# Performance work log

Measured on AMD Instinct MI355X. Metric: run time of the kernel, lower is better.

## Reference

```python
import jax, jax.numpy as jnp
import numpy as np

T, D, H, E, K = 8192, 1024, 1024, 8, 2
N = T * K  # total dispatched rows


def setup_inputs() -> dict:
    key = jax.random.key(0)
    ks = jax.random.split(key, 12)
    s = 1.0 / np.sqrt(D)
    inp = {
        # uniform, contiguous per-expert segments: 2048 rows each
        'offsets': jnp.arange(E + 1, dtype=jnp.int64 if jax.config.jax_enable_x64 else jnp.int32) * (N // E),
        'jagged': jax.random.normal(ks[0], (T, D), jnp.float32),
        'weight': jax.random.normal(ks[1], (E, D, H), jnp.float32) * s,
        'bias': jax.random.normal(ks[2], (E, H), jnp.float32) * 0.02,
        'index': jax.random.randint(ks[3], (N,), 0, T),
        'weight_p': jax.random.normal(ks[4], (E, D, H), jnp.float32) * s,
        'weight_out': jax.random.normal(ks[5], (E, H, D), jnp.float32) * (1.0 / np.sqrt(H)),
        'reverse_index': jax.random.randint(ks[6], (T, K), 0, N),
        'gates': jax.random.uniform(ks[7], (N,), jnp.float32),
        'gates_index': jax.random.randint(ks[8], (T, K), 0, N),
        'bias_p': jax.random.normal(ks[9], (E, H), jnp.float32) * 0.02,
        'bias_out': jax.random.normal(ks[10], (E, D), jnp.float32) * 0.02,
    }
    return inp


def reference(offsets, jagged, weight, bias, index, weight_p, weight_out,
              reverse_index, gates, gates_index, bias_p, bias_out):
    # dispatch: gather token features into expert-sorted order  [N, D]
    x = jagged[index]
    n = x.shape[0]
    n_experts = weight.shape[0]
    # contiguous segment id per dispatched row
    expert_id = jnp.searchsorted(offsets, jnp.arange(n), side='right') - 1
    y = jnp.zeros((n, weight_out.shape[-1]), dtype=x.dtype)
    for e in range(n_experts):  # fixed small expert count
        m = (expert_id == e)[:, None].astype(x.dtype)
        xe = x * m
        g = xe @ weight[e] + bias[e]        # gate proj  [N, H]
        u = xe @ weight_p[e] + bias_p[e]    # up proj    [N, H]
        h = jax.nn.silu(g) * u              # SwiGLU
        y = y + (h @ weight_out[e] + bias_out[e]) * m
    # combine: gather K expert outputs per token, weight by gates  [T, D]
    gathered = y[reverse_index]             # [T, K, D]
    gv = gates[gates_index]                 # [T, K]
    return jnp.einsum('tkd,tk->td', gathered, gv)
```

## Files before the change

kernel.cpp:

```cpp
#include <hip/hip_runtime.h>
#include <hip/hip_bf16.h>

#define T_TOK 8192
#define DDIM 1024
#define HDIM 1024
#define NEXP 8
#define KTOP 2
#define NROWS (T_TOK * KTOP)

typedef __attribute__((ext_vector_type(8))) short bf16x8;
typedef __attribute__((ext_vector_type(8))) unsigned short u16x8;
typedef __attribute__((ext_vector_type(4))) float f32x4;

__device__ __forceinline__ unsigned short f2bf(float f) {
    unsigned u = __builtin_bit_cast(unsigned, f);
    u += 0x7fffu + ((u >> 16) & 1u);
    return (unsigned short)(u >> 16);
}
__device__ __forceinline__ float bf2f(unsigned short h) {
    return __builtin_bit_cast(float, (unsigned)h << 16);
}

__device__ __forceinline__ void gll16(const unsigned short* g, const unsigned short* l) {
    __builtin_amdgcn_global_load_lds(
        (const __attribute__((address_space(1))) unsigned int*)g,
        (__attribute__((address_space(3))) unsigned int*)l, 16, 0, 0);
}


__global__ __launch_bounds__(256) void cvt_bf16_k(const float* __restrict__ in,
                                                  unsigned short* __restrict__ out, int n4) {
    int i = blockIdx.x * 256 + threadIdx.x;
    if (i >= n4) return;
    float4 v = ((const float4*)in)[i];
    ushort4 o;
    o.x = f2bf(v.x); o.y = f2bf(v.y); o.z = f2bf(v.z); o.w = f2bf(v.w);
    ((ushort4*)out)[i] = o;
}

__global__ __launch_bounds__(256) void transpose_cast3_k(
    const float* __restrict__ w1, const float* __restrict__ w2,
    const float* __restrict__ w3, unsigned short* __restrict__ o1,
    unsigned short* __restrict__ o2, unsigned short* __restrict__ o3) {
    __shared__ float tile[64][65];
    int z = blockIdx.z;
    int which = z >> 3, m = z & 7;
    const float* src = (which == 0 ? w1 : which == 1 ? w2 : w3) + (size_t)m * DDIM * HDIM;
    unsigned short* dst = (which == 0 ? o1 : which == 1 ? o2 : o3) + (size_t)m * DDIM * HDIM;
    int c0 = blockIdx.x * 64, r0 = blockIdx.y * 64;
    int t = threadIdx.x;
    int rr = t >> 4;
    int cc = (t & 15) * 4;
#pragma unroll
    for (int p = 0; p < 4; ++p) {
        float4 v = *(const float4*)&src[(size_t)(r0 + rr + p * 16) * HDIM + c0 + cc];
        tile[rr + p * 16][cc]     = v.x;
        tile[rr + p * 16][cc + 1] = v.y;
        tile[rr + p * 16][cc + 2] = v.z;
        tile[rr + p * 16][cc + 3] = v.w;
    }
    __syncthreads();
    int rb = (t & 7) * 8;
    int oc = t >> 3;
#pragma unroll
    for (int q = 0; q < 2; ++q) {
        int c = oc + q * 32;
        u16x8 o;
#pragma unroll
        for (int j = 0; j < 8; ++j)
            o[j] = f2bf(tile[rb + j][c]);
        *(u16x8*)&dst[(size_t)(c0 + c) * DDIM + r0 + rb] = o;
    }
}


constexpr int BMk = 128, BNk = 128, BKk = 64;

__global__ __launch_bounds__(256, 2) void gemm128_fused_k(
    const unsigned short* __restrict__ A, const int* __restrict__ rowidx,
    const unsigned short* __restrict__ B1t, const unsigned short* __restrict__ B2t,
    const float* __restrict__ b1E, const float* __restrict__ b2E,
    unsigned short* __restrict__ Out, const int* __restrict__ offsets) {
    const int N = HDIM, K = DDIM, lda = DDIM;
    __shared__ __attribute__((aligned(16))) unsigned short lds[24576];

    const int nbn = N / BNk;
    int l = (blockIdx.x & 7) * 128 + (blockIdx.x >> 3);
    int brow = l / nbn, bcol = l % nbn;
    int row0 = brow * BMk, col0 = bcol * BNk;
    int e = 0;
    while (offsets[e + 1] <= row0) ++e;

    const unsigned short* B1e = B1t + (size_t)e * N * K;
    const unsigned short* B2e = B2t + (size_t)e * N * K;
    const float* b1 = b1E + (size_t)e * N;
    const float* b2 = b2E + (size_t)e * N;

    int tid = threadIdx.x;
    int lane = tid & 63, wid = tid >> 6;
    int wr = wid >> 1, wc = wid & 1;
    int l15 = lane & 15, l4 = lane >> 4;

    int srow = lane >> 3;
    int c8 = ((lane & 7) ^ srow) * 8;
    const unsigned short* aS[4];
    const unsigned short* b1S[4];
    const unsigned short* b2S[4];
#pragma unroll
    for (int q = 0; q < 4; ++q) {
        int g = wid * 4 + q;
        int gr = row0 + g * 8 + srow;
        aS[q]  = A + (size_t)rowidx[gr] * lda + c8;
        b1S[q] = B1e + (size_t)(col0 + g * 8 + srow) * K + c8;
        b2S[q] = B2e + (size_t)(col0 + g * 8 + srow) * K + c8;
    }

    const char* LB = (const char*)lds;
    int arow = (wr * 64 + l15) * 128;
    int brw = (wc * 64 + l15) * 128;
    int cx = l15 & 7;
    int ch0 = (l4 ^ cx) * 16;
    int ch1 = ((4 + l4) ^ cx) * 16;

    f32x4 acc1[4][4] = {};
    f32x4 acc2[4][4] = {};

#pragma unroll 1
    for (int t = 0; t < K / BKk; ++t) {
        int k0 = t * BKk;
#pragma unroll
        for (int q = 0; q < 4; ++q) {
            gll16(aS[q] + k0,  lds + (wid * 4 + q) * 512);
            gll16(b1S[q] + k0, lds + 8192 + (wid * 4 + q) * 512);
            gll16(b2S[q] + k0, lds + 16384 + (wid * 4 + q) * 512);
        }
        __syncthreads();
#pragma unroll
        for (int s = 0; s < 2; ++s) {
            int ch = s ? ch1 : ch0;
            bf16x8 fa[4], fb1[4], fb2[4];
#pragma unroll
            for (int mi = 0; mi < 4; ++mi)
                fa[mi] = *(const bf16x8*)(LB + arow + mi * 2048 + ch);
#pragma unroll
            for (int ni = 0; ni < 4; ++ni) {
                fb1[ni] = *(const bf16x8*)(LB + 8192 * 2 + brw + ni * 2048 + ch);
                fb2[ni] = *(const bf16x8*)(LB + 8192 * 4 + brw + ni * 2048 + ch);
            }
#pragma unroll
            for (int mi = 0; mi < 4; ++mi)
#pragma unroll
                for (int ni = 0; ni < 4; ++ni) {
                    acc1[mi][ni] = __builtin_amdgcn_mfma_f32_16x16x32_bf16(
                        fa[mi], fb1[ni], acc1[mi][ni], 0, 0, 0);
                    acc2[mi][ni] = __builtin_amdgcn_mfma_f32_16x16x32_bf16(
                        fa[mi], fb2[ni], acc2[mi][ni], 0, 0, 0);
                }
        }
        __syncthreads();
    }

    float bv1[4], bv2[4];
#pragma unroll
    for (int ni = 0; ni < 4; ++ni) {
        int c = col0 + wc * 64 + ni * 16 + l15;
        bv1[ni] = b1[c];
        bv2[ni] = b2[c];
    }

#pragma unroll
    for (int mi = 0; mi < 4; ++mi) {
        int orow_b = row0 + wr * 64 + mi * 16 + l4 * 4;
#pragma unroll
        for (int ni = 0; ni < 4; ++ni) {
            int ocol = col0 + wc * 64 + ni * 16 + l15;
#pragma unroll
            for (int q = 0; q < 4; ++q) {
                float g = acc1[mi][ni][q] + bv1[ni];
                float u = acc2[mi][ni][q] + bv2[ni];
                float s = g / (1.0f + __expf(-g));
                Out[(size_t)(orow_b + q) * N + ocol] = f2bf(s * u);
            }
        }
    }
}

__global__ __launch_bounds__(256, 4) void gemm128_k(
    const unsigned short* __restrict__ A, int lda,
    const unsigned short* __restrict__ Bt, const float* __restrict__ biasE,
    unsigned short* __restrict__ Out, const int* __restrict__ offsets,
    int N, int K) {
    __shared__ __attribute__((aligned(16))) unsigned short lds[16384];

    const int nbn = N / BNk;
    int l = (blockIdx.x & 7) * 128 + (blockIdx.x >> 3);
    int brow = l / nbn, bcol = l % nbn;
    int row0 = brow * BMk, col0 = bcol * BNk;
    int e = 0;
    while (offsets[e + 1] <= row0) ++e;

    const unsigned short* Bte = Bt + (size_t)e * N * K;
    const float* bias = biasE + (size_t)e * N;

    int tid = threadIdx.x;
    int lane = tid & 63, wid = tid >> 6;
    int wr = wid >> 1, wc = wid & 1;
    int l15 = lane & 15, l4 = lane >> 4;

    int srow = lane >> 3;
    int c8 = ((lane & 7) ^ srow) * 8;
    const unsigned short* aS[4];
    const unsigned short* bS[4];
#pragma unroll
    for (int q = 0; q < 4; ++q) {
        int g = wid * 4 + q;
        aS[q] = A + (size_t)(row0 + g * 8 + srow) * lda + c8;
        bS[q] = Bte + (size_t)(col0 + g * 8 + srow) * K + c8;
    }

    const char* LB = (const char*)lds;
    int arow = (wr * 64 + l15) * 128;
    int brw = (wc * 64 + l15) * 128;
    int cx = l15 & 7;
    int ch0 = (l4 ^ cx) * 16;
    int ch1 = ((4 + l4) ^ cx) * 16;

    f32x4 acc[4][4] = {};

#pragma unroll 1
    for (int t = 0; t < K / BKk; ++t) {
        int k0 = t * BKk;
#pragma unroll
        for (int q = 0; q < 4; ++q) {
            gll16(aS[q] + k0, lds + (wid * 4 + q) * 512);
            gll16(bS[q] + k0, lds + 8192 + (wid * 4 + q) * 512);
        }
        __syncthreads();
        bf16x8 fa[2][4], fb[2][4];
#pragma unroll
        for (int mi = 0; mi < 4; ++mi) {
            fa[0][mi] = *(const bf16x8*)(LB + arow + mi * 2048 + ch0);
            fa[1][mi] = *(const bf16x8*)(LB + arow + mi * 2048 + ch1);
        }
#pragma unroll
        for (int ni = 0; ni < 4; ++ni) {
            fb[0][ni] = *(const bf16x8*)(LB + 16384 + brw + ni * 2048 + ch0);
            fb[1][ni] = *(const bf16x8*)(LB + 16384 + brw + ni * 2048 + ch1);
        }
#pragma unroll
        for (int s = 0; s < 2; ++s)
#pragma unroll
            for (int mi = 0; mi < 4; ++mi)
#pragma unroll
                for (int ni = 0; ni < 4; ++ni)
                    acc[mi][ni] = __builtin_amdgcn_mfma_f32_16x16x32_bf16(
                        fa[s][mi], fb[s][ni], acc[mi][ni], 0, 0, 0);
        __syncthreads();
    }

    float bv[4];
#pragma unroll
    for (int ni = 0; ni < 4; ++ni)
        bv[ni] = bias[col0 + wc * 64 + ni * 16 + l15];

#pragma unroll
    for (int mi = 0; mi < 4; ++mi) {
        int orow_b = row0 + wr * 64 + mi * 16 + l4 * 4;
#pragma unroll
        for (int ni = 0; ni < 4; ++ni) {
            int ocol = col0 + wc * 64 + ni * 16 + l15;
#pragma unroll
            for (int q = 0; q < 4; ++q)
                Out[(size_t)(orow_b + q) * N + ocol] = f2bf(acc[mi][ni][q] + bv[ni]);
        }
    }
}


__global__ __launch_bounds__(256) void combine_k(
    const unsigned short* __restrict__ Y, const int* __restrict__ rev,
    const float* __restrict__ gates, const int* __restrict__ gidx,
    float* __restrict__ out) {
    int t = blockIdx.x;
    int r0 = rev[2 * t], r1 = rev[2 * t + 1];
    float g0 = gates[gidx[2 * t]], g1 = gates[gidx[2 * t + 1]];
    const unsigned short* y0 = Y + (size_t)r0 * DDIM;
    const unsigned short* y1 = Y + (size_t)r1 * DDIM;
    int d = threadIdx.x * 4;
    ushort4 a = *(const ushort4*)(y0 + d);
    ushort4 b = *(const ushort4*)(y1 + d);
    float4 r;
    r.x = g0 * bf2f(a.x) + g1 * bf2f(b.x);
    r.y = g0 * bf2f(a.y) + g1 * bf2f(b.y);
    r.z = g0 * bf2f(a.z) + g1 * bf2f(b.z);
    r.w = g0 * bf2f(a.w) + g1 * bf2f(b.w);
    *(float4*)(out + (size_t)t * DDIM + d) = r;
}


extern "C" void kernel_launch(void* const* d_in, const int* in_sizes, int n_in,
                              void* d_out, int out_size, void* d_ws, size_t ws_size,
                              hipStream_t stream) {
    const int* offsets = (const int*)d_in[0];
    const float* jagged = (const float*)d_in[1];
    const float* weight = (const float*)d_in[2];
    const float* bias = (const float*)d_in[3];
    const int* index = (const int*)d_in[4];
    const float* weight_p = (const float*)d_in[5];
    const float* weight_out = (const float*)d_in[6];
    const int* rev = (const int*)d_in[7];
    const float* gates = (const float*)d_in[8];
    const int* gidx = (const int*)d_in[9];
    const float* bias_p = (const float*)d_in[10];
    const float* bias_out = (const float*)d_in[11];
    float* out = (float*)d_out;

    char* w = (char*)d_ws;
    unsigned short* jag_bf = (unsigned short*)w; w += (size_t)T_TOK * DDIM * 2;
    unsigned short* W1t    = (unsigned short*)w; w += (size_t)NEXP * DDIM * HDIM * 2;
    unsigned short* Wpt    = (unsigned short*)w; w += (size_t)NEXP * DDIM * HDIM * 2;
    unsigned short* Wot    = (unsigned short*)w; w += (size_t)NEXP * HDIM * DDIM * 2;
    unsigned short* h_ws   = (unsigned short*)w; w += (size_t)NROWS * HDIM * 2;
    unsigned short* y_ws   = (unsigned short*)w; w += (size_t)NROWS * DDIM * 2;

    cvt_bf16_k<<<(T_TOK * DDIM / 4 + 255) / 256, 256, 0, stream>>>(jagged, jag_bf, T_TOK * DDIM / 4);
    transpose_cast3_k<<<dim3(HDIM / 64, DDIM / 64, 3 * NEXP), 256, 0, stream>>>(
        weight, weight_p, weight_out, W1t, Wpt, Wot);

    const int grid = (NROWS / BMk) * (HDIM / BNk);

    gemm128_fused_k<<<grid, 256, 0, stream>>>(jag_bf, index, W1t, Wpt, bias, bias_p,
                                              h_ws, offsets);
    gemm128_k<<<grid, 256, 0, stream>>>(h_ws, HDIM, Wot, bias_out, y_ws,
                                        offsets, DDIM, HDIM);
    combine_k<<<T_TOK, 256, 0, stream>>>(y_ws, rev, gates, gidx, out);
}
```

Before: 157.9 us.

## Use 256-row tiles in down-projection GEMM to reuse B fragments across two row halves

The second (down-projection) GEMM now computes a 256x128 output tile per block by loading two 128-row A slabs and one B slab per k-step. Each B fragment is used for two sets of MFMAs, which halves B traffic from global memory and LDS per output element. In exchange the block uses more LDS and twice the accumulator registers, launch bounds drop to 2 blocks per SM, and the grid halves to 512 blocks, which may cut occupancy and latency hiding. The expert lookup still uses row0, and since segments are 2048 rows, a 256-row tile stays within one expert.

```diff
diff --git a/kernel.cpp b/kernel.cpp
--- a/kernel.cpp
+++ b/kernel.cpp
@@ -185,17 +185,18 @@
     }
 }
 
-__global__ __launch_bounds__(256, 4) void gemm128_k(
+
+__global__ __launch_bounds__(256, 2) void gemm128_dualrow_k(
     const unsigned short* __restrict__ A, int lda,
     const unsigned short* __restrict__ Bt, const float* __restrict__ biasE,
     unsigned short* __restrict__ Out, const int* __restrict__ offsets,
     int N, int K) {
-    __shared__ __attribute__((aligned(16))) unsigned short lds[16384];
+    __shared__ __attribute__((aligned(16))) unsigned short lds[24576];
 
     const int nbn = N / BNk;
-    int l = (blockIdx.x & 7) * 128 + (blockIdx.x >> 3);
+    int l = (blockIdx.x & 7) * 64 + (blockIdx.x >> 3);
     int brow = l / nbn, bcol = l % nbn;
-    int row0 = brow * BMk, col0 = bcol * BNk;
+    int row0 = brow * 256, col0 = bcol * BNk;
     int e = 0;
     while (offsets[e + 1] <= row0) ++e;
 
@@ -209,13 +210,15 @@
 
     int srow = lane >> 3;
     int c8 = ((lane & 7) ^ srow) * 8;
-    const unsigned short* aS[4];
+    const unsigned short* a1S[4];
+    const unsigned short* a2S[4];
     const unsigned short* bS[4];
 #pragma unroll
     for (int q = 0; q < 4; ++q) {
         int g = wid * 4 + q;
-        aS[q] = A + (size_t)(row0 + g * 8 + srow) * lda + c8;
-        bS[q] = Bte + (size_t)(col0 + g * 8 + srow) * K + c8;
+        a1S[q] = A + (size_t)(row0 + g * 8 + srow) * lda + c8;
+        a2S[q] = A + (size_t)(row0 + 128 + g * 8 + srow) * lda + c8;
+        bS[q]  = Bte + (size_t)(col0 + g * 8 + srow) * K + c8;
     }
 
     const char* LB = (const char*)lds;
@@ -225,36 +228,41 @@
     int ch0 = (l4 ^ cx) * 16;
     int ch1 = ((4 + l4) ^ cx) * 16;
 
-    f32x4 acc[4][4] = {};
+    f32x4 acc1[4][4] = {};
+    f32x4 acc2[4][4] = {};
 
 #pragma unroll 1
     for (int t = 0; t < K / BKk; ++t) {
         int k0 = t * BKk;
 #pragma unroll
         for (int q = 0; q < 4; ++q) {
-            gll16(aS[q] + k0, lds + (wid * 4 + q) * 512);
-            gll16(bS[q] + k0, lds + 8192 + (wid * 4 + q) * 512);
+            gll16(a1S[q] + k0, lds + (wid * 4 + q) * 512);
+            gll16(a2S[q] + k0, lds + 8192 + (wid * 4 + q) * 512);
+            gll16(bS[q] + k0,  lds + 16384 + (wid * 4 + q) * 512);
         }
         __syncthreads();
-        bf16x8 fa[2][4], fb[2][4];
-#pragma unroll
-        for (int mi = 0; mi < 4; ++mi) {
-            fa[0][mi] = *(const bf16x8*)(LB + arow + mi * 2048 + ch0);
-            fa[1][mi] = *(const bf16x8*)(LB + arow + mi * 2048 + ch1);
-        }
-#pragma unroll
-        for (int ni = 0; ni < 4; ++ni) {
-            fb[0][ni] = *(const bf16x8*)(LB + 16384 + brw + ni * 2048 + ch0);
-            fb[1][ni] = *(const bf16x8*)(LB + 16384 + brw + ni * 2048 + ch1);
-        }
-#pragma unroll
-        for (int s = 0; s < 2; ++s)
+#pragma unroll
+        for (int s = 0; s < 2; ++s) {
+            int ch = s ? ch1 : ch0;
+            bf16x8 fa1[4], fa2[4], fb[4];
+#pragma unroll
+            for (int mi = 0; mi < 4; ++mi) {
+                fa1[mi] = *(const bf16x8*)(LB + arow + mi * 2048 + ch);
+                fa2[mi] = *(const bf16x8*)(LB + 16384 + arow + mi * 2048 + ch);
+            }
+#pragma unroll
+            for (int ni = 0; ni < 4; ++ni)
+                fb[ni] = *(const bf16x8*)(LB + 32768 + brw + ni * 2048 + ch);
 #pragma unroll
             for (int mi = 0; mi < 4; ++mi)
 #pragma unroll
-                for (int ni = 0; ni < 4; ++ni)
-                    acc[mi][ni] = __builtin_amdgcn_mfma_f32_16x16x32_bf16(
-                        fa[s][mi], fb[s][ni], acc[mi][ni], 0, 0, 0);
+                for (int ni = 0; ni < 4; ++ni) {
+                    acc1[mi][ni] = __builtin_amdgcn_mfma_f32_16x16x32_bf16(
+                        fa1[mi], fb[ni], acc1[mi][ni], 0, 0, 0);
+                    acc2[mi][ni] = __builtin_amdgcn_mfma_f32_16x16x32_bf16(
+                        fa2[mi], fb[ni], acc2[mi][ni], 0, 0, 0);
+                }
+        }
         __syncthreads();
     }
 
@@ -265,13 +273,16 @@
 
 #pragma unroll
     for (int mi = 0; mi < 4; ++mi) {
-        int orow_b = row0 + wr * 64 + mi * 16 + l4 * 4;
+        int orow1 = row0 + wr * 64 + mi * 16 + l4 * 4;
+        int orow2 = orow1 + 128;
 #pragma unroll
         for (int ni = 0; ni < 4; ++ni) {
             int ocol = col0 + wc * 64 + ni * 16 + l15;
 #pragma unroll
-            for (int q = 0; q < 4; ++q)
-                Out[(size_t)(orow_b + q) * N + ocol] = f2bf(acc[mi][ni][q] + bv[ni]);
+            for (int q = 0; q < 4; ++q) {
+                Out[(size_t)(orow1 + q) * N + ocol] = f2bf(acc1[mi][ni][q] + bv[ni]);
+                Out[(size_t)(orow2 + q) * N + ocol] = f2bf(acc2[mi][ni][q] + bv[ni]);
+            }
         }
     }
 }
@@ -331,7 +342,8 @@
 
     gemm128_fused_k<<<grid, 256, 0, stream>>>(jag_bf, index, W1t, Wpt, bias, bias_p,
                                               h_ws, offsets);
-    gemm128_k<<<grid, 256, 0, stream>>>(h_ws, HDIM, Wot, bias_out, y_ws,
-                                        offsets, DDIM, HDIM);
+    const int grid_y = (NROWS / 256) * (DDIM / BNk);
+    gemm128_dualrow_k<<<grid_y, 256, 0, stream>>>(h_ws, HDIM, Wot, bias_out, y_ws,
+                                                  offsets, DDIM, HDIM);
     combine_k<<<T_TOK, 256, 0, stream>>>(y_ws, rev, gates, gidx, out);
 }
```

Result: no change. 155.0 us (median of 2 runs) (-1.9%).
